# Performance work log

Measured on AMD Instinct MI355X. Metric: run time of the kernel, lower is better.

The kernel has to match this reference:

```python
import jax, jax.numpy as jnp
import numpy as np

# AWLoss config (matches init_kwargs): method='fft', filter_dim=2, filter_scale=2,
# mode='reverse', reduction='sum', epsilon=1e-9 (pre-whitening), std=1e-4, eta=0, gamma=0
EPSILON = 1e-9
STD = 1e-4
DIMS = (-2, -1)          # self.dims for filter_dim=2
FS = (3, 511, 511)       # get_filter_shape([B,3,256,256]): [nc, 2H-1, 2W-1]


def pad_signal(x, shape):
    # center-pad dims 1.. of x up to `shape` (extra sample on the right).
    pads = [(0, 0)]
    for i, s in enumerate(shape):
        p1 = (s - x.shape[i + 1]) // 2
        pads.append((p1, s - x.shape[i + 1] - p1))
    return jnp.pad(x, pads)


def make_penalty(shape, std):
    # inverted multivariate gaussian on [-1,1]^d grid: 0 at center, ->1 away
    axes = [jnp.linspace(-1.0, 1.0, n) for n in shape]
    mesh = jnp.stack(jnp.meshgrid(*axes, indexing='ij'), axis=-1)  # (h, w, 2)
    d = mesh.shape[-1]
    logp = -0.5 * jnp.sum((mesh / std) ** 2, axis=-1) \
           - 0.5 * d * jnp.log(2.0 * jnp.pi * std * std)
    rv = jnp.exp(logp)
    rv = rv / jnp.max(jnp.abs(rv))
    return -rv + jnp.max(rv)  # eta=0 => no random additive term


def wienerfft(x, y, fs, prwh):
    # least-squares Wiener filter transforming x into y, via FFT
    Fx_flip = jnp.fft.fftn(jnp.flip(x, DIMS), axes=DIMS)
    Fccorr = Fx_flip * jnp.fft.fftn(y, axes=DIMS)   # cross-correlation spectrum
    Facorr = Fx_flip * jnp.fft.fftn(x, axes=DIMS)   # auto-correlation spectrum
    Fdconv = (Fccorr + prwh) / (Facorr + prwh)      # regularized deconvolution
    # irfftn crops last axis to fs[-1]//2+1 (numpy/torch semantics match)
    rolled = jnp.fft.irfftn(Fdconv, s=fs[-2:], axes=DIMS)
    # roll: int(-n/2)-1 per trailing dim (n odd => -(n//2)-1)
    shifts = tuple(-(x.shape[i] // 2) - 1 for i in range(1, x.ndim))[-2:]
    return jnp.roll(rolled, shifts, axis=DIMS)


def awloss(recon, target):
    fs = FS
    recon_p = pad_signal(recon, fs)   # [B, C, 511, 511]
    target_p = pad_signal(target, fs)
    # mode='reverse': filter transforms target into recon
    x, y = target_p, recon_p
    v = wienerfft(x, y, fs, EPSILON)                       # [B, C, 511, 511]
    vnorm = jnp.sqrt(jnp.sum(v * v, axis=DIMS, keepdims=True))
    v = v / vnorm                                          # unit-energy filter
    T = make_penalty(fs[-2:], STD)                         # (511, 511)
    f = 0.5 * jnp.sum((T * v) ** 2)                        # reduction='sum'
    return f


def setup_inputs() -> dict:
    key = jax.random.key(0)
    k1, k2 = jax.random.split(key)
    recon = jax.random.normal(k1, (16, 3, 256, 256), dtype=jnp.float32)
    target = jax.random.normal(k2, (16, 3, 256, 256), dtype=jnp.float32)
    return {"recon": recon, "target": target}


def reference(recon, target):
    return awloss(recon, target)
```

## Files before the change

kernel.cpp:

```cpp
#include <hip/hip_runtime.h>
#include <math.h>


#define NCH 48
#define PADOFF 127
#define TWO_PI_F 6.283185307179586f

typedef float f32x4 __attribute__((ext_vector_type(4)));
typedef short s16x8 __attribute__((ext_vector_type(8)));
typedef unsigned short u16;

union frag_u { u16 u[8]; s16x8 v; };

__device__ __forceinline__ u16 f2bf(float f) {
    union { float f; unsigned u; } x; x.f = f;
    unsigned r = x.u + 0x7FFFu + ((x.u >> 16) & 1u);
    return (u16)(r >> 16);
}

#define MFMA16(A, B, C) __builtin_amdgcn_mfma_f32_16x16x32_bf16(A, B, C, 0, 0, 0)

__global__ __launch_bounds__(256) void setup(u16* __restrict__ w2f,
                                             float* __restrict__ sacc) {
    __shared__ float cs[511], sn[511];
    int tid = threadIdx.x;
    for (int i = tid; i < 511; i += 256) {
        float a = -TWO_PI_F * (float)i / 511.0f;
        cs[i] = cosf(a);
        sn[i] = sinf(a);
    }
    __syncthreads();

    int i = blockIdx.x * 256 + tid;
    int j = i & 7, l = (i >> 3) & 63, kk = (i >> 9) & 7;
    int c = (i >> 12) & 1, kt = i >> 13;
    int k1 = 16 * kt + (l & 15);
    u16 v = 0;
    if (k1 < 511) {
        int n = 32 * kk + 8 * (l >> 4) + j;
        int p = (k1 * (n + PADOFF)) % 511;
        v = f2bf(c ? sn[p] : cs[p]);
    }
    w2f[i] = v;
    if (blockIdx.x == 0 && tid < 2 * NCH) sacc[tid] = 0.0f;
}

__global__ __launch_bounds__(256, 2) void stage1(const float* __restrict__ target,
                                                 const float* __restrict__ recon,
                                                 const u16* __restrict__ w2f,
                                                 u16* __restrict__ x1t,
                                                 int c0) {
    int tid = threadIdx.x;
    int w = tid >> 6, l = tid & 63;
    int lm = l & 15, lh = l >> 4;
    int h   = blockIdx.x & 1;
    int q   = (blockIdx.x >> 1) & 3;
    int imgl = blockIdx.x >> 3;
    int lc = imgl >> 1;
    int tsel = imgl & 1;
    const float* src = (tsel == 0 ? target : recon) + (size_t)(c0 + lc) * 65536;
    int r0 = 64 * q;

    __shared__ u16 lin[16384];

    {
        int row = tid >> 2;
        int cg  = tid & 3;
        const float* rp = src + (size_t)(r0 + row) * 256 + cg * 64;
        float4 v[16];
        #pragma unroll
        for (int i = 0; i < 16; ++i) v[i] = *(const float4*)(rp + 4 * i);
        u16 b[64];
        #pragma unroll
        for (int i = 0; i < 16; ++i) {
            b[4*i]   = f2bf(v[i].x); b[4*i+1] = f2bf(v[i].y);
            b[4*i+2] = f2bf(v[i].z); b[4*i+3] = f2bf(v[i].w);
        }
        int s = row >> 4, lmw = row & 15;
        #pragma unroll
        for (int i2 = 0; i2 < 8; ++i2) {
            int col0 = cg * 64 + i2 * 8;
            int kk = col0 >> 5, lhw = (col0 >> 3) & 3;
            u16* dst = &lin[((s * 8 + kk) * 512) + (lhw * 16 + lmw) * 8];
            *(s16x8*)dst = *(const s16x8*)&b[i2 * 8];
        }
    }

    int t0 = 8 * h + 2 * w;
    s16x8 tw00[8], tw01[8], tw10[8], tw11[8];
    {
        const u16* p0 = w2f + (size_t)t0 * 8192 + l * 8;
        const u16* p1 = w2f + (size_t)(t0 + 1) * 8192 + l * 8;
        #pragma unroll
        for (int kk = 0; kk < 8; ++kk) {
            tw00[kk] = *(const s16x8*)(p0 + kk * 512);
            tw01[kk] = *(const s16x8*)(p0 + 4096 + kk * 512);
            tw10[kk] = *(const s16x8*)(p1 + kk * 512);
            tw11[kk] = *(const s16x8*)(p1 + 4096 + kk * 512);
        }
    }
    __syncthreads();

    f32x4 a00[4], a01[4], a10[4], a11[4];
    #pragma unroll
    for (int s = 0; s < 4; ++s) {
        a00[s] = (f32x4){0,0,0,0}; a01[s] = (f32x4){0,0,0,0};
        a10[s] = (f32x4){0,0,0,0}; a11[s] = (f32x4){0,0,0,0};
    }
    #pragma unroll
    for (int kk = 0; kk < 8; ++kk) {
        s16x8 af[4];
        #pragma unroll
        for (int s = 0; s < 4; ++s)
            af[s] = *(const s16x8*)&lin[((s * 8 + kk) * 512) + l * 8];
        #pragma unroll
        for (int s = 0; s < 4; ++s) {
            a00[s] = MFMA16(af[s], tw00[kk], a00[s]);
            a01[s] = MFMA16(af[s], tw01[kk], a01[s]);
            a10[s] = MFMA16(af[s], tw10[kk], a10[s]);
            a11[s] = MFMA16(af[s], tw11[kk], a11[s]);
        }
    }

    u16* chdst = x1t + (size_t)(lc * 4 + tsel * 2) * 65536;
    #pragma unroll
    for (int s = 0; s < 4; ++s) {
        size_t off0 = (size_t)(16 * t0 + lm) * 256 + r0 + 16 * s + 4 * lh;
        size_t off1 = off0 + 4096;
        ushort4 o;
        o.x = f2bf(a00[s][0]); o.y = f2bf(a00[s][1]);
        o.z = f2bf(a00[s][2]); o.w = f2bf(a00[s][3]);
        *(ushort4*)(chdst + off0) = o;
        o.x = f2bf(a01[s][0]); o.y = f2bf(a01[s][1]);
        o.z = f2bf(a01[s][2]); o.w = f2bf(a01[s][3]);
        *(ushort4*)(chdst + 65536 + off0) = o;
        o.x = f2bf(a10[s][0]); o.y = f2bf(a10[s][1]);
        o.z = f2bf(a10[s][2]); o.w = f2bf(a10[s][3]);
        *(ushort4*)(chdst + off1) = o;
        o.x = f2bf(a11[s][0]); o.y = f2bf(a11[s][1]);
        o.z = f2bf(a11[s][2]); o.w = f2bf(a11[s][3]);
        *(ushort4*)(chdst + 65536 + off1) = o;
    }
}

__global__ __launch_bounds__(256)
__attribute__((amdgpu_waves_per_eu(1, 1)))
void stage2(const u16* __restrict__ x1t,
            const u16* __restrict__ w2f,
            float* __restrict__ sacc,
            int c0, int cc) {
    int tid = threadIdx.x;
    int w = tid >> 6, l = tid & 63;
    int lm = l & 15, lh = l >> 4;
    int task = blockIdx.x * 4 + w;
    int lc = task >> 4;
    int t  = task & 15;

    const u16* base = x1t + (size_t)(4 * lc) * 65536;
    size_t roff = (size_t)(16 * t + lm) * 256 + 8 * lh;

    s16x8 ar[8], ai[8], br[8], bi[8];
    #pragma unroll
    for (int kk = 0; kk < 8; ++kk) {
        size_t off = roff + 32 * kk;
        ar[kk] = *(const s16x8*)(base + off);
        ai[kk] = *(const s16x8*)(base + 65536 + off);
        br[kk] = *(const s16x8*)(base + 131072 + off);
        bi[kk] = *(const s16x8*)(base + 196608 + off);
    }
    #pragma unroll
    for (int kk = 0; kk < 8; ++kk)
        asm volatile("" : "+v"(ar[kk]), "+v"(ai[kk]), "+v"(br[kk]), "+v"(bi[kk]));

    int k2 = 16 * t + lm;
    float wgt = (k2 == 0) ? 1.f : 2.f;
    float s1 = 0.f, s2 = 0.f;

#define LOADW(WR, WI, KT) do {                                              \
    const u16* wp_ = w2f + (size_t)(KT) * 8192 + l * 8;                     \
    _Pragma("unroll")                                                       \
    for (int kk = 0; kk < 8; ++kk) {                                        \
        WR[kk] = *(const s16x8*)(wp_ + kk * 512);                           \
        WI[kk] = *(const s16x8*)(wp_ + 4096 + kk * 512);                    \
    } } while (0)

#define COMPUTE(WR, WI, KT) do {                                            \
    f32x4 crr = {0,0,0,0}, cii = {0,0,0,0}, cri = {0,0,0,0}, cir = {0,0,0,0}; \
    f32x4 drr = {0,0,0,0}, dii = {0,0,0,0}, dri = {0,0,0,0}, dir = {0,0,0,0}; \
    _Pragma("unroll")                                                       \
    for (int kk = 0; kk < 8; ++kk) {                                        \
        crr = MFMA16(WR[kk], ar[kk], crr);                                  \
        cii = MFMA16(WI[kk], ai[kk], cii);                                  \
        cri = MFMA16(WR[kk], ai[kk], cri);                                  \
        cir = MFMA16(WI[kk], ar[kk], cir);                                  \
        drr = MFMA16(WR[kk], br[kk], drr);                                  \
        dii = MFMA16(WI[kk], bi[kk], dii);                                  \
        dri = MFMA16(WR[kk], bi[kk], dri);                                  \
        dir = MFMA16(WI[kk], br[kk], dir);                                  \
    }                                                                       \
    _Pragma("unroll")                                                       \
    for (int r = 0; r < 4; ++r) {                                           \
        int k1_ = 16 * (KT) + 4 * lh + r;                                   \
        float wg2 = (k1_ < 511) ? wgt : 0.f;                                \
        float Xr = crr[r] - cii[r], Xi = cri[r] + cir[r];                   \
        float Yr = drr[r] - dii[r], Yi = dri[r] + dir[r];                   \
        float Pr = Xr * Yr + Xi * Yi;                                       \
        float Pi = Xr * Yi - Xi * Yr;                                       \
        float Q  = Xr * Xr + Xi * Xi;                                       \
        float inv = 1.0f / (Q * Q + 1e-30f);                                \
        s1 += wg2 * Pr * Q * inv;                                           \
        s2 += wg2 * (Pr * Pr + Pi * Pi) * inv;                              \
    } } while (0)

    s16x8 wrA[8], wiA[8], wrB[8], wiB[8];
    LOADW(wrA, wiA, 0);
    for (int kt = 0; kt < 32; kt += 2) {
        LOADW(wrB, wiB, kt + 1);
        COMPUTE(wrA, wiA, kt);
        if (kt + 2 < 32) LOADW(wrA, wiA, kt + 2);
        COMPUTE(wrB, wiB, kt + 1);
    }
#undef LOADW
#undef COMPUTE

    #pragma unroll
    for (int off = 32; off > 0; off >>= 1) {
        s1 += __shfl_down(s1, off);
        s2 += __shfl_down(s2, off);
    }
    if (l == 0) {
        atomicAdd(&sacc[c0 + lc], s1);
        atomicAdd(&sacc[NCH + c0 + lc], s2);
    }
}

__global__ void finalize(const float* __restrict__ s, float* __restrict__ out) {
    int t = threadIdx.x;
    float v = 0.f;
    if (t < NCH) {
        float s1 = s[t], s2 = s[NCH + t];
        v = (s2 != 0.f) ? (s1 * s1) / s2 : 0.f;
    }
    for (int off = 32; off > 0; off >>= 1) v += __shfl_down(v, off);
    if (t == 0) out[0] = 24.0f - 0.5f * v / 261121.0f;
}

extern "C" void kernel_launch(void* const* d_in, const int* in_sizes, int n_in,
                              void* d_out, int out_size, void* d_ws, size_t ws_size,
                              hipStream_t stream) {
    const float* recon  = (const float*)d_in[0];
    const float* target = (const float*)d_in[1];
    float* out = (float*)d_out;
    char* ws = (char*)d_ws;

    const size_t OFF_W2F = 0;
    const size_t OFF_S   = OFF_W2F + 524288;
    const size_t OFF_X1  = OFF_S + 512;

    u16*   w2f  = (u16*)(ws + OFF_W2F);
    float* sacc = (float*)(ws + OFF_S);
    u16*   x1t  = (u16*)(ws + OFF_X1);

    const size_t perch = 4ull * 65536 * 2;
    size_t avail = (ws_size > OFF_X1) ? ws_size - OFF_X1 : 0;
    int chunk = (int)(avail / perch);
    if (chunk > NCH) chunk = NCH;
    if (chunk < 1) chunk = 1;

    setup<<<dim3(1024), dim3(256), 0, stream>>>(w2f, sacc);

    for (int c0 = 0; c0 < NCH; c0 += chunk) {
        int cc = (NCH - c0 < chunk) ? (NCH - c0) : chunk;
        stage1<<<dim3(16 * cc), dim3(256), 0, stream>>>(target, recon, w2f, x1t, c0);
        stage2<<<dim3(cc * 4), dim3(256), 0, stream>>>(x1t, w2f, sacc, c0, cc);
    }
    finalize<<<dim3(1), dim3(64), 0, stream>>>(sacc, out);
}
```

Measured before the change: 71.13 us.

## Split stage2 k-tiles across eight waves sharing LDS-staged input fragments

Stage2 now runs one 512-thread block per (channel, row-tile) task. The 32 output k-tiles are split across 8 waves, 4 per wave, where before one wave looped over all 32. The shared input fragments are loaded once per block into LDS with global_load_lds and then read into registers by every wave. This raises parallelism fourfold (16*cc blocks instead of 4*cc) and removes redundant global loads. It gives up the explicit double-buffered weight prefetch and the waves_per_eu(1,1) hint, and the block reduction now issues more atomics per channel.

```diff
diff --git a/kernel.cpp b/kernel.cpp
--- a/kernel.cpp
+++ b/kernel.cpp
@@ -9,6 +9,9 @@
 typedef float f32x4 __attribute__((ext_vector_type(4)));
 typedef short s16x8 __attribute__((ext_vector_type(8)));
 typedef unsigned short u16;
+
+typedef __attribute__((address_space(1))) const unsigned char* gas_p;
+typedef __attribute__((address_space(3))) unsigned char* las_p;
 
 union frag_u { u16 u[8]; s16x8 v; };
 
@@ -143,30 +146,36 @@
     }
 }
 
-__global__ __launch_bounds__(256)
-__attribute__((amdgpu_waves_per_eu(1, 1)))
-void stage2(const u16* __restrict__ x1t,
-            const u16* __restrict__ w2f,
-            float* __restrict__ sacc,
-            int c0, int cc) {
+__global__ __launch_bounds__(512) void stage2(const u16* __restrict__ x1t,
+                                              const u16* __restrict__ w2f,
+                                              float* __restrict__ sacc,
+                                              int c0, int cc) {
     int tid = threadIdx.x;
     int w = tid >> 6, l = tid & 63;
     int lm = l & 15, lh = l >> 4;
-    int task = blockIdx.x * 4 + w;
-    int lc = task >> 4;
-    int t  = task & 15;
-
-    const u16* base = x1t + (size_t)(4 * lc) * 65536;
-    size_t roff = (size_t)(16 * t + lm) * 256 + 8 * lh;
+    int lc = blockIdx.x >> 4;
+    int t  = blockIdx.x & 15;
+
+    __shared__ u16 fbuf[16384];
+
+    const u16* cb = x1t + (size_t)(4 * lc) * 65536;
+    int rowoff = (16 * t + lm) * 256 + 8 * lh;
+    #pragma unroll
+    for (int q = 0; q < 4; ++q) {
+        int pair = w * 4 + q;
+        int p = pair >> 3, kk = pair & 7;
+        const u16* g = cb + (size_t)p * 65536 + rowoff + 32 * kk;
+        __builtin_amdgcn_global_load_lds((gas_p)g, (las_p)&fbuf[pair * 512], 16, 0, 0);
+    }
+    __syncthreads();
 
     s16x8 ar[8], ai[8], br[8], bi[8];
     #pragma unroll
     for (int kk = 0; kk < 8; ++kk) {
-        size_t off = roff + 32 * kk;
-        ar[kk] = *(const s16x8*)(base + off);
-        ai[kk] = *(const s16x8*)(base + 65536 + off);
-        br[kk] = *(const s16x8*)(base + 131072 + off);
-        bi[kk] = *(const s16x8*)(base + 196608 + off);
+        ar[kk] = *(const s16x8*)&fbuf[(0 * 8 + kk) * 512 + l * 8];
+        ai[kk] = *(const s16x8*)&fbuf[(1 * 8 + kk) * 512 + l * 8];
+        br[kk] = *(const s16x8*)&fbuf[(2 * 8 + kk) * 512 + l * 8];
+        bi[kk] = *(const s16x8*)&fbuf[(3 * 8 + kk) * 512 + l * 8];
     }
     #pragma unroll
     for (int kk = 0; kk < 8; ++kk)
@@ -176,52 +185,38 @@
     float wgt = (k2 == 0) ? 1.f : 2.f;
     float s1 = 0.f, s2 = 0.f;
 
-#define LOADW(WR, WI, KT) do {                                              \
-    const u16* wp_ = w2f + (size_t)(KT) * 8192 + l * 8;                     \
-    _Pragma("unroll")                                                       \
-    for (int kk = 0; kk < 8; ++kk) {                                        \
-        WR[kk] = *(const s16x8*)(wp_ + kk * 512);                           \
-        WI[kk] = *(const s16x8*)(wp_ + 4096 + kk * 512);                    \
-    } } while (0)
-
-#define COMPUTE(WR, WI, KT) do {                                            \
-    f32x4 crr = {0,0,0,0}, cii = {0,0,0,0}, cri = {0,0,0,0}, cir = {0,0,0,0}; \
-    f32x4 drr = {0,0,0,0}, dii = {0,0,0,0}, dri = {0,0,0,0}, dir = {0,0,0,0}; \
-    _Pragma("unroll")                                                       \
-    for (int kk = 0; kk < 8; ++kk) {                                        \
-        crr = MFMA16(WR[kk], ar[kk], crr);                                  \
-        cii = MFMA16(WI[kk], ai[kk], cii);                                  \
-        cri = MFMA16(WR[kk], ai[kk], cri);                                  \
-        cir = MFMA16(WI[kk], ar[kk], cir);                                  \
-        drr = MFMA16(WR[kk], br[kk], drr);                                  \
-        dii = MFMA16(WI[kk], bi[kk], dii);                                  \
-        dri = MFMA16(WR[kk], bi[kk], dri);                                  \
-        dir = MFMA16(WI[kk], br[kk], dir);                                  \
-    }                                                                       \
-    _Pragma("unroll")                                                       \
-    for (int r = 0; r < 4; ++r) {                                           \
-        int k1_ = 16 * (KT) + 4 * lh + r;                                   \
-        float wg2 = (k1_ < 511) ? wgt : 0.f;                                \
-        float Xr = crr[r] - cii[r], Xi = cri[r] + cir[r];                   \
-        float Yr = drr[r] - dii[r], Yi = dri[r] + dir[r];                   \
-        float Pr = Xr * Yr + Xi * Yi;                                       \
-        float Pi = Xr * Yi - Xi * Yr;                                       \
-        float Q  = Xr * Xr + Xi * Xi;                                       \
-        float inv = 1.0f / (Q * Q + 1e-30f);                                \
-        s1 += wg2 * Pr * Q * inv;                                           \
-        s2 += wg2 * (Pr * Pr + Pi * Pi) * inv;                              \
-    } } while (0)
-
-    s16x8 wrA[8], wiA[8], wrB[8], wiB[8];
-    LOADW(wrA, wiA, 0);
-    for (int kt = 0; kt < 32; kt += 2) {
-        LOADW(wrB, wiB, kt + 1);
-        COMPUTE(wrA, wiA, kt);
-        if (kt + 2 < 32) LOADW(wrA, wiA, kt + 2);
-        COMPUTE(wrB, wiB, kt + 1);
-    }
-#undef LOADW
-#undef COMPUTE
+    for (int i = 0; i < 4; ++i) {
+        int kt = 4 * w + i;
+        const u16* wp = w2f + (size_t)kt * 8192 + l * 8;
+        f32x4 crr = {0,0,0,0}, cii = {0,0,0,0}, cri = {0,0,0,0}, cir = {0,0,0,0};
+        f32x4 drr = {0,0,0,0}, dii = {0,0,0,0}, dri = {0,0,0,0}, dir = {0,0,0,0};
+        #pragma unroll
+        for (int kk = 0; kk < 8; ++kk) {
+            s16x8 wr = *(const s16x8*)(wp + kk * 512);
+            s16x8 wi = *(const s16x8*)(wp + 4096 + kk * 512);
+            crr = MFMA16(wr, ar[kk], crr);
+            cii = MFMA16(wi, ai[kk], cii);
+            cri = MFMA16(wr, ai[kk], cri);
+            cir = MFMA16(wi, ar[kk], cir);
+            drr = MFMA16(wr, br[kk], drr);
+            dii = MFMA16(wi, bi[kk], dii);
+            dri = MFMA16(wr, bi[kk], dri);
+            dir = MFMA16(wi, br[kk], dir);
+        }
+        #pragma unroll
+        for (int r = 0; r < 4; ++r) {
+            int k1 = 16 * kt + 4 * lh + r;
+            float wg2 = (k1 < 511) ? wgt : 0.f;
+            float Xr = crr[r] - cii[r], Xi = cri[r] + cir[r];
+            float Yr = drr[r] - dii[r], Yi = dri[r] + dir[r];
+            float Pr = Xr * Yr + Xi * Yi;
+            float Pi = Xr * Yi - Xi * Yr;
+            float Q  = Xr * Xr + Xi * Xi;
+            float inv = 1.0f / (Q * Q + 1e-30f);
+            s1 += wg2 * Pr * Q * inv;
+            s2 += wg2 * (Pr * Pr + Pi * Pi) * inv;
+        }
+    }
 
     #pragma unroll
     for (int off = 32; off > 0; off >>= 1) {
@@ -272,7 +267,7 @@
     for (int c0 = 0; c0 < NCH; c0 += chunk) {
         int cc = (NCH - c0 < chunk) ? (NCH - c0) : chunk;
         stage1<<<dim3(16 * cc), dim3(256), 0, stream>>>(target, recon, w2f, x1t, c0);
-        stage2<<<dim3(cc * 4), dim3(256), 0, stream>>>(x1t, w2f, sacc, c0, cc);
+        stage2<<<dim3(16 * cc), dim3(512), 0, stream>>>(x1t, w2f, sacc, c0, cc);
     }
     finalize<<<dim3(1), dim3(64), 0, stream>>>(sacc, out);
 }
```

After: 112.6 us. 58.3% more time.
